# Optimization experiments

Hardware: AMD Instinct MI355X
Metric: run time of the kernel (lower is better)

Reference implementation:

```python
import jax, jax.numpy as jnp
import numpy as np

B = 4096      # batch (number of graphs / query nodes)
N = 524288    # total ball nodes (~128 per graph)
H = 128       # hidden_dim


def setup_inputs() -> dict:
    key = jax.random.key(0)
    ks = jax.random.split(key, 12)
    s = 0.05
    return {
        "query": jax.random.normal(ks[0], (B, H), dtype=jnp.float32),
        "ball": jax.random.normal(ks[1], (N, H), dtype=jnp.float32),
        "ball_batch": jnp.sort(jax.random.randint(ks[2], (N,), 0, B, dtype=jnp.int32)),
        # ball_attention: Linear(H, H//2) -> Tanh -> Linear(H//2, 1)
        "attn_w1": jax.random.normal(ks[3], (H, H // 2), dtype=jnp.float32) * s,
        "attn_b1": jnp.zeros((H // 2,), dtype=jnp.float32),
        "attn_w2": jax.random.normal(ks[4], (H // 2, 1), dtype=jnp.float32) * s,
        "attn_b2": jnp.zeros((1,), dtype=jnp.float32),
        # combiner: Linear(2H, H) -> LayerNorm(H) -> GELU
        "comb_w": jax.random.normal(ks[5], (2 * H, H), dtype=jnp.float32) * s,
        "comb_b": jnp.zeros((H,), dtype=jnp.float32),
        "ln_g": jnp.ones((H,), dtype=jnp.float32),
        "ln_b": jnp.zeros((H,), dtype=jnp.float32),
        # boundary head: Linear(H, H//2) -> ReLU -> Linear(H//2, 1)
        "bnd_w1": jax.random.normal(ks[6], (H, H // 2), dtype=jnp.float32) * s,
        "bnd_b1": jnp.zeros((H // 2,), dtype=jnp.float32),
        "bnd_w2": jax.random.normal(ks[7], (H // 2, 1), dtype=jnp.float32) * s,
        "bnd_b2": jnp.zeros((1,), dtype=jnp.float32),
        # wicket head: Linear(H, H//2) -> ReLU -> Linear(H//2, 1)
        "wkt_w1": jax.random.normal(ks[8], (H, H // 2), dtype=jnp.float32) * s,
        "wkt_b1": jnp.zeros((H // 2,), dtype=jnp.float32),
        "wkt_w2": jax.random.normal(ks[9], (H // 2, 1), dtype=jnp.float32) * s,
        "wkt_b2": jnp.zeros((1,), dtype=jnp.float32),
    }


def reference(query, ball, ball_batch, attn_w1, attn_b1, attn_w2, attn_b2,
              comb_w, comb_b, ln_g, ln_b,
              bnd_w1, bnd_b1, bnd_w2, bnd_b2,
              wkt_w1, wkt_b1, wkt_w2, wkt_b2):
    nb = query.shape[0]  # static batch size
    # attention score MLP over ball nodes -> [N]
    scores = (jnp.tanh(ball @ attn_w1 + attn_b1) @ attn_w2 + attn_b2)[:, 0]
    # segment softmax (stable: subtract per-segment max)
    seg_max = jax.ops.segment_max(scores, ball_batch, num_segments=nb)
    e = jnp.exp(scores - seg_max[ball_batch])
    denom = jax.ops.segment_sum(e, ball_batch, num_segments=nb)
    w = e / denom[ball_batch]
    # weighted-sum pooling -> [B, H]
    pooled = jax.ops.segment_sum(w[:, None] * ball, ball_batch, num_segments=nb)
    # concat + combiner: Linear -> LayerNorm -> GELU (exact, torch default)
    h = jnp.concatenate([query, pooled], axis=-1) @ comb_w + comb_b
    mu = jnp.mean(h, axis=-1, keepdims=True)
    var = jnp.mean((h - mu) ** 2, axis=-1, keepdims=True)
    h = (h - mu) / jnp.sqrt(var + 1e-5) * ln_g + ln_b
    h = jax.nn.gelu(h, approximate=False)
    boundary = jax.nn.relu(h @ bnd_w1 + bnd_b1) @ bnd_w2 + bnd_b2
    wicket = jax.nn.relu(h @ wkt_w1 + wkt_b1) @ wkt_w2 + wkt_b2
    return boundary, wicket
```

## Files before the change

kernel.cpp:

```cpp
#include <hip/hip_runtime.h>
#include <math.h>

#define N_NODES 524288
#define BATCH   4096
#define HID     128
#define MAXL    512

typedef __attribute__((ext_vector_type(8))) short bf16x8;
typedef __attribute__((ext_vector_type(4))) float f32x4;

__device__ __forceinline__ unsigned short f2bf(float f) {
  unsigned int u = __float_as_uint(f);
  u = (u + 0x7FFFu + ((u >> 16) & 1u)) >> 16;
  return (unsigned short)u;
}

__device__ __forceinline__ float fast_tanh(float x) {
  float cx = fminf(fmaxf(x, -9.f), 9.f);
  float e  = __expf(2.f * cx);
  return (e - 1.f) * __builtin_amdgcn_rcpf(e + 1.f);
}

__global__ __launch_bounds__(256) void k_bounds(const int* __restrict__ bb,
                                                int* __restrict__ rs)
{
  const int i = blockIdx.x * 256 + threadIdx.x;
  if (i >= N_NODES) return;
  const int cur  = bb[i];
  const int prev = (i == 0) ? -1 : bb[i - 1];
  for (int b = prev + 1; b <= cur; ++b) rs[b] = i;
  if (i == N_NODES - 1)
    for (int b = cur + 1; b <= BATCH; ++b) rs[b] = N_NODES;
}

__global__ __launch_bounds__(256, 8) void k_score_pool(
    const float* __restrict__ ball, const int* __restrict__ rs,
    const float* __restrict__ w1, const float* __restrict__ b1,
    const float* __restrict__ w2, const float* __restrict__ b2,
    float* __restrict__ pooled)
{
  __shared__ float  s_part[4][MAXL];
  __shared__ float  s_red[4];
  __shared__ float4 s_red4[3][32];

  const int tid  = threadIdx.x;
  const int lane = tid & 63;
  const int wv   = tid >> 6;
  const int m16  = lane & 15;
  const int quad = lane >> 4;
  const int b    = blockIdx.x;

  const int start = rs[b];
  const int end   = rs[b + 1];
  int L = end - start;

  float4* outp = (float4*)(pooled + (size_t)b * HID);
  if (L <= 0) { if (tid < 32) outp[tid] = make_float4(0.f,0.f,0.f,0.f); return; }
  if (L > MAXL) L = MAXL;

  bf16x8 fb[4];
  const int n = wv * 16 + m16;
  #pragma unroll
  for (int s = 0; s < 4; ++s) {
    const int k0 = s * 32 + quad * 8;
    bf16x8 v;
    #pragma unroll
    for (int j = 0; j < 8; ++j) v[j] = (short)f2bf(w1[(k0 + j) * 64 + n]);
    fb[s] = v;
  }
  const float b1v = b1[n], w2v = w2[n];

  for (int t0 = 0; t0 < L; t0 += 16) {
    int row = start + t0 + m16;
    if (row >= end) row = end - 1;
    const float4* rp = (const float4*)(ball + (size_t)row * HID) + quad * 2;
    f32x4 acc = {0.f, 0.f, 0.f, 0.f};
    #pragma unroll
    for (int s = 0; s < 4; ++s) {
      float4 x0 = rp[s * 8], x1 = rp[s * 8 + 1];
      bf16x8 fa;
      fa[0]=(short)f2bf(x0.x); fa[1]=(short)f2bf(x0.y);
      fa[2]=(short)f2bf(x0.z); fa[3]=(short)f2bf(x0.w);
      fa[4]=(short)f2bf(x1.x); fa[5]=(short)f2bf(x1.y);
      fa[6]=(short)f2bf(x1.z); fa[7]=(short)f2bf(x1.w);
      acc = __builtin_amdgcn_mfma_f32_16x16x32_bf16(fa, fb[s], acc, 0,0,0);
    }
    #pragma unroll
    for (int r = 0; r < 4; ++r) {
      float p = fast_tanh(acc[r] + b1v) * w2v;
      p += __shfl_xor(p, 1); p += __shfl_xor(p, 2);
      p += __shfl_xor(p, 4); p += __shfl_xor(p, 8);
      const int idx = t0 + quad * 4 + r;
      if (m16 == 0 && idx < L) s_part[wv][idx] = p;
    }
    __syncthreads();
  }
  __syncthreads();

  float m = -INFINITY;
  for (int i = lane; i < L; i += 64)
    m = fmaxf(m, s_part[0][i] + s_part[1][i] + s_part[2][i] + s_part[3][i]);
  #pragma unroll
  for (int o = 32; o; o >>= 1) m = fmaxf(m, __shfl_xor(m, o));
  __syncthreads();

  float d = 0.f;
  for (int i = wv * 64 + lane; i < L; i += 256) {
    float e = __expf(s_part[0][i] + s_part[1][i] + s_part[2][i] + s_part[3][i] - m);
    s_part[0][i] = e;
    d += e;
  }
  #pragma unroll
  for (int o = 32; o; o >>= 1) d += __shfl_xor(d, o);
  if (lane == 0) s_red[wv] = d;
  __syncthreads();
  const float inv = __builtin_amdgcn_rcpf(s_red[0] + s_red[1] + s_red[2] + s_red[3]);

  const int lh = lane >> 5;
  const int c4 = lane & 31;
  float4 acc = {0.f, 0.f, 0.f, 0.f};
  #pragma unroll 4
  for (int i = start + wv * 2; i + 1 < end; i += 8) {
    const int   row = i + lh;
    const float w   = s_part[0][row - start];
    const float4 v  = ((const float4*)(ball + (size_t)row * HID))[c4];
    acc.x = fmaf(w, v.x, acc.x);
    acc.y = fmaf(w, v.y, acc.y);
    acc.z = fmaf(w, v.z, acc.z);
    acc.w = fmaf(w, v.w, acc.w);
  }
  if ((L & 1) && wv == 0 && lh == 0) {
    const int   row = end - 1;
    const float w   = s_part[0][row - start];
    const float4 v  = ((const float4*)(ball + (size_t)row * HID))[c4];
    acc.x = fmaf(w, v.x, acc.x);
    acc.y = fmaf(w, v.y, acc.y);
    acc.z = fmaf(w, v.z, acc.z);
    acc.w = fmaf(w, v.w, acc.w);
  }
  acc.x += __shfl_xor(acc.x, 32);
  acc.y += __shfl_xor(acc.y, 32);
  acc.z += __shfl_xor(acc.z, 32);
  acc.w += __shfl_xor(acc.w, 32);
  if (wv != 0) { if (lh == 0) s_red4[wv - 1][c4] = acc; }
  __syncthreads();
  if (wv == 0 && lh == 0) {
    const float4 a1 = s_red4[0][c4], a2 = s_red4[1][c4], a3 = s_red4[2][c4];
    float4 o;
    o.x = (acc.x + a1.x + a2.x + a3.x) * inv;
    o.y = (acc.y + a1.y + a2.y + a3.y) * inv;
    o.z = (acc.z + a1.z + a2.z + a3.z) * inv;
    o.w = (acc.w + a1.w + a2.w + a3.w) * inv;
    outp[c4] = o;
  }
}

__global__ __launch_bounds__(128) void k_combine(
    const float* __restrict__ query, const float* __restrict__ pooled,
    const float* __restrict__ cw, const float* __restrict__ cb,
    const float* __restrict__ lg, const float* __restrict__ lb,
    const float* __restrict__ bw1, const float* __restrict__ bb1,
    const float* __restrict__ bw2, const float* __restrict__ bb2,
    const float* __restrict__ ww1, const float* __restrict__ wb1,
    const float* __restrict__ ww2, const float* __restrict__ wb2,
    float* __restrict__ out)
{
  __shared__ float in_lds[256][8];
  __shared__ float h_lds[128][8];
  __shared__ float part[2][2][8];
  const int tid  = threadIdx.x;
  const int row0 = blockIdx.x * 8;

  for (int idx = tid; idx < 2048; idx += 128) {
    const int k = idx >> 3, r = idx & 7;
    float v = (k < 128) ? query[(size_t)(row0 + r) * 128 + k]
                        : pooled[(size_t)(row0 + r) * 128 + (k - 128)];
    in_lds[k][r] = v;
  }
  __syncthreads();

  const int j = tid;
  float acc[8];
  const float cbj = cb[j];
  #pragma unroll
  for (int r = 0; r < 8; ++r) acc[r] = cbj;
  for (int k = 0; k < 256; ++k) {
    const float w = cw[k * 128 + j];
    #pragma unroll
    for (int r = 0; r < 8; ++r) acc[r] = fmaf(in_lds[k][r], w, acc[r]);
  }

  const int wv = tid >> 6, ln = tid & 63;
  #pragma unroll
  for (int r = 0; r < 8; ++r) {
    float v = acc[r], v2 = v * v;
    #pragma unroll
    for (int o = 32; o; o >>= 1) { v += __shfl_xor(v, o); v2 += __shfl_xor(v2, o); }
    if (ln == 0) { part[0][wv][r] = v; part[1][wv][r] = v2; }
  }
  __syncthreads();
  const float gj = lg[j], bj = lb[j];
  #pragma unroll
  for (int r = 0; r < 8; ++r) {
    const float S = part[0][0][r] + part[0][1][r];
    const float Q = part[1][0][r] + part[1][1][r];
    const float mean = S * (1.f / 128.f);
    const float var  = Q * (1.f / 128.f) - mean * mean;
    const float rs   = rsqrtf(var + 1e-5f);
    float x = (acc[r] - mean) * rs * gj + bj;
    x = 0.5f * x * (1.f + erff(x * 0.70710678118654752f));
    h_lds[j][r] = x;
  }
  __syncthreads();

  const float* W1 = wv ? ww1 : bw1;
  const float* B1 = wv ? wb1 : bb1;
  const float* W2 = wv ? ww2 : bw2;
  const float  B2 = wv ? wb2[0] : bb2[0];
  float t[8];
  const float b1l = B1[ln];
  #pragma unroll
  for (int r = 0; r < 8; ++r) t[r] = b1l;
  for (int k = 0; k < 128; ++k) {
    const float w = W1[k * 64 + ln];
    #pragma unroll
    for (int r = 0; r < 8; ++r) t[r] = fmaf(h_lds[k][r], w, t[r]);
  }
  const float w2l = W2[ln];
  #pragma unroll
  for (int r = 0; r < 8; ++r) {
    float o = fmaxf(t[r], 0.f) * w2l;
    #pragma unroll
    for (int m = 32; m; m >>= 1) o += __shfl_xor(o, m);
    if (ln == 0) out[wv * BATCH + row0 + r] = o + B2;
  }
}

extern "C" void kernel_launch(void* const* d_in, const int* in_sizes, int n_in,
                              void* d_out, int out_size, void* d_ws, size_t ws_size,
                              hipStream_t stream)
{
  const float* query = (const float*)d_in[0];
  const float* ball  = (const float*)d_in[1];
  const int*   bb    = (const int*)  d_in[2];
  const float* aw1   = (const float*)d_in[3];
  const float* ab1   = (const float*)d_in[4];
  const float* aw2   = (const float*)d_in[5];
  const float* ab2   = (const float*)d_in[6];
  const float* cw    = (const float*)d_in[7];
  const float* cb    = (const float*)d_in[8];
  const float* lg    = (const float*)d_in[9];
  const float* lbeta = (const float*)d_in[10];
  const float* bw1   = (const float*)d_in[11];
  const float* bb1   = (const float*)d_in[12];
  const float* bw2   = (const float*)d_in[13];
  const float* bb2   = (const float*)d_in[14];
  const float* ww1   = (const float*)d_in[15];
  const float* wb1   = (const float*)d_in[16];
  const float* ww2   = (const float*)d_in[17];
  const float* wb2   = (const float*)d_in[18];

  float* pooled = (float*)d_ws;
  int*   rs     = (int*)(pooled + (size_t)BATCH * HID);
  float* out    = (float*)d_out;

  k_bounds<<<(N_NODES + 255) / 256, 256, 0, stream>>>(bb, rs);
  k_score_pool<<<BATCH, 256, 0, stream>>>(ball, rs, aw1, ab1, aw2, ab2, pooled);
  k_combine<<<BATCH / 8, 128, 0, stream>>>(query, pooled, cw, cb, lg, lbeta,
                                           bw1, bb1, bw2, bb2, ww1, wb1, ww2, wb2, out);
}
```

Baseline: 488.2 us.

## Stage ball rows in swizzled LDS with double buffering and online softmax

Restructures the score+pool kernel so each segment's ball rows are loaded from global memory once, in 32-row chunks, into a double-buffered, XOR-swizzled LDS tile. Both the MFMA scoring and the weighted pooling read from that tile, with an online running-max softmax replacing the separate max/sum/pool passes. This removes the second global read of every ball row and the MAXL cap on segment length. In exchange it uses about 32KB of LDS per block, which lowers occupancy, and adds extra barriers per chunk.

```diff
diff --git a/kernel.cpp b/kernel.cpp
--- a/kernel.cpp
+++ b/kernel.cpp
@@ -4,7 +4,7 @@
 #define N_NODES 524288
 #define BATCH   4096
 #define HID     128
-#define MAXL    512
+#define CH      32
 
 typedef __attribute__((ext_vector_type(8))) short bf16x8;
 typedef __attribute__((ext_vector_type(4))) float f32x4;
@@ -20,6 +20,8 @@
   float e  = __expf(2.f * cx);
   return (e - 1.f) * __builtin_amdgcn_rcpf(e + 1.f);
 }
+
+#define SWZ(row, col) (((row) * HID) + ((((col) >> 2) ^ ((row) & 7)) << 2) + ((col) & 3))
 
 __global__ __launch_bounds__(256) void k_bounds(const int* __restrict__ bb,
                                                 int* __restrict__ rs)
@@ -33,15 +35,16 @@
     for (int b = cur + 1; b <= BATCH; ++b) rs[b] = N_NODES;
 }
 
-__global__ __launch_bounds__(256, 8) void k_score_pool(
+__global__ __launch_bounds__(256) void k_score_pool(
     const float* __restrict__ ball, const int* __restrict__ rs,
     const float* __restrict__ w1, const float* __restrict__ b1,
     const float* __restrict__ w2, const float* __restrict__ b2,
     float* __restrict__ pooled)
 {
-  __shared__ float  s_part[4][MAXL];
-  __shared__ float  s_red[4];
-  __shared__ float4 s_red4[3][32];
+  __shared__ __align__(16) float buf[2][CH * HID];
+  __shared__ float s_part[4][CH];
+  __shared__ float s_red[4];
+  __shared__ float s_obuf[3][HID];
 
   const int tid  = threadIdx.x;
   const int lane = tid & 63;
@@ -52,11 +55,10 @@
 
   const int start = rs[b];
   const int end   = rs[b + 1];
-  int L = end - start;
-
-  float4* outp = (float4*)(pooled + (size_t)b * HID);
-  if (L <= 0) { if (tid < 32) outp[tid] = make_float4(0.f,0.f,0.f,0.f); return; }
-  if (L > MAXL) L = MAXL;
+  const int L     = end - start;
+
+  float2* outp = (float2*)(pooled + (size_t)b * HID);
+  if (L <= 0) { if (tid < 64) outp[tid] = make_float2(0.f, 0.f); return; }
 
   bf16x8 fb[4];
   const int n = wv * 16 + m16;
@@ -70,88 +72,107 @@
   }
   const float b1v = b1[n], w2v = w2[n];
 
-  for (int t0 = 0; t0 < L; t0 += 16) {
-    int row = start + t0 + m16;
-    if (row >= end) row = end - 1;
-    const float4* rp = (const float4*)(ball + (size_t)row * HID) + quad * 2;
-    f32x4 acc = {0.f, 0.f, 0.f, 0.f};
-    #pragma unroll
-    for (int s = 0; s < 4; ++s) {
-      float4 x0 = rp[s * 8], x1 = rp[s * 8 + 1];
-      bf16x8 fa;
-      fa[0]=(short)f2bf(x0.x); fa[1]=(short)f2bf(x0.y);
-      fa[2]=(short)f2bf(x0.z); fa[3]=(short)f2bf(x0.w);
-      fa[4]=(short)f2bf(x1.x); fa[5]=(short)f2bf(x1.y);
-      fa[6]=(short)f2bf(x1.z); fa[7]=(short)f2bf(x1.w);
-      acc = __builtin_amdgcn_mfma_f32_16x16x32_bf16(fa, fb[s], acc, 0,0,0);
-    }
-    #pragma unroll
-    for (int r = 0; r < 4; ++r) {
-      float p = fast_tanh(acc[r] + b1v) * w2v;
-      p += __shfl_xor(p, 1); p += __shfl_xor(p, 2);
-      p += __shfl_xor(p, 4); p += __shfl_xor(p, 8);
-      const int idx = t0 + quad * 4 + r;
-      if (m16 == 0 && idx < L) s_part[wv][idx] = p;
+  const int nc = (L + CH - 1) / CH;
+  float4 pre[4];
+
+  #pragma unroll
+  for (int rnd = 0; rnd < 4; ++rnd) {
+    const int f = rnd * 1024 + tid * 4;
+    const int row = f >> 7, col = f & 127;
+    int gr = start + row; if (gr >= end) gr = end - 1;
+    pre[rnd] = *(const float4*)(ball + (size_t)gr * HID + col);
+  }
+  #pragma unroll
+  for (int rnd = 0; rnd < 4; ++rnd) {
+    const int f = rnd * 1024 + tid * 4;
+    const int row = f >> 7, col = f & 127;
+    *(float4*)&buf[0][SWZ(row, col)] = pre[rnd];
+  }
+  __syncthreads();
+
+  float  m_run = -INFINITY, d_run = 0.f;
+  float2 O = make_float2(0.f, 0.f);
+  int p = 0;
+
+  for (int c = 0; c < nc; ++c) {
+    const int Lc = min(CH, L - c * CH);
+
+    if (c + 1 < nc) {
+      #pragma unroll
+      for (int rnd = 0; rnd < 4; ++rnd) {
+        const int f = rnd * 1024 + tid * 4;
+        const int row = f >> 7, col = f & 127;
+        int gr = start + (c + 1) * CH + row; if (gr >= end) gr = end - 1;
+        pre[rnd] = *(const float4*)(ball + (size_t)gr * HID + col);
+      }
+    }
+
+    #pragma unroll
+    for (int sub = 0; sub < 2; ++sub) {
+      const int row = sub * 16 + m16;
+      f32x4 acc = {0.f, 0.f, 0.f, 0.f};
+      #pragma unroll
+      for (int s = 0; s < 4; ++s) {
+        const float4 x0 = *(const float4*)&buf[p][SWZ(row, s * 32 + quad * 8)];
+        const float4 x1 = *(const float4*)&buf[p][SWZ(row, s * 32 + quad * 8 + 4)];
+        bf16x8 fa;
+        fa[0]=(short)f2bf(x0.x); fa[1]=(short)f2bf(x0.y);
+        fa[2]=(short)f2bf(x0.z); fa[3]=(short)f2bf(x0.w);
+        fa[4]=(short)f2bf(x1.x); fa[5]=(short)f2bf(x1.y);
+        fa[6]=(short)f2bf(x1.z); fa[7]=(short)f2bf(x1.w);
+        acc = __builtin_amdgcn_mfma_f32_16x16x32_bf16(fa, fb[s], acc, 0,0,0);
+      }
+      #pragma unroll
+      for (int r = 0; r < 4; ++r) {
+        float sc = fast_tanh(acc[r] + b1v) * w2v;
+        sc += __shfl_xor(sc, 1); sc += __shfl_xor(sc, 2);
+        sc += __shfl_xor(sc, 4); sc += __shfl_xor(sc, 8);
+        if (m16 == 0) s_part[wv][sub * 16 + quad * 4 + r] = sc;
+      }
     }
     __syncthreads();
-  }
-  __syncthreads();
-
-  float m = -INFINITY;
-  for (int i = lane; i < L; i += 64)
-    m = fmaxf(m, s_part[0][i] + s_part[1][i] + s_part[2][i] + s_part[3][i]);
-  #pragma unroll
-  for (int o = 32; o; o >>= 1) m = fmaxf(m, __shfl_xor(m, o));
-  __syncthreads();
-
-  float d = 0.f;
-  for (int i = wv * 64 + lane; i < L; i += 256) {
-    float e = __expf(s_part[0][i] + s_part[1][i] + s_part[2][i] + s_part[3][i] - m);
-    s_part[0][i] = e;
-    d += e;
-  }
-  #pragma unroll
-  for (int o = 32; o; o >>= 1) d += __shfl_xor(d, o);
-  if (lane == 0) s_red[wv] = d;
-  __syncthreads();
-  const float inv = __builtin_amdgcn_rcpf(s_red[0] + s_red[1] + s_red[2] + s_red[3]);
-
-  const int lh = lane >> 5;
-  const int c4 = lane & 31;
-  float4 acc = {0.f, 0.f, 0.f, 0.f};
-  #pragma unroll 4
-  for (int i = start + wv * 2; i + 1 < end; i += 8) {
-    const int   row = i + lh;
-    const float w   = s_part[0][row - start];
-    const float4 v  = ((const float4*)(ball + (size_t)row * HID))[c4];
-    acc.x = fmaf(w, v.x, acc.x);
-    acc.y = fmaf(w, v.y, acc.y);
-    acc.z = fmaf(w, v.z, acc.z);
-    acc.w = fmaf(w, v.w, acc.w);
-  }
-  if ((L & 1) && wv == 0 && lh == 0) {
-    const int   row = end - 1;
-    const float w   = s_part[0][row - start];
-    const float4 v  = ((const float4*)(ball + (size_t)row * HID))[c4];
-    acc.x = fmaf(w, v.x, acc.x);
-    acc.y = fmaf(w, v.y, acc.y);
-    acc.z = fmaf(w, v.z, acc.z);
-    acc.w = fmaf(w, v.w, acc.w);
-  }
-  acc.x += __shfl_xor(acc.x, 32);
-  acc.y += __shfl_xor(acc.y, 32);
-  acc.z += __shfl_xor(acc.z, 32);
-  acc.w += __shfl_xor(acc.w, 32);
-  if (wv != 0) { if (lh == 0) s_red4[wv - 1][c4] = acc; }
-  __syncthreads();
-  if (wv == 0 && lh == 0) {
-    const float4 a1 = s_red4[0][c4], a2 = s_red4[1][c4], a3 = s_red4[2][c4];
-    float4 o;
-    o.x = (acc.x + a1.x + a2.x + a3.x) * inv;
-    o.y = (acc.y + a1.y + a2.y + a3.y) * inv;
-    o.z = (acc.z + a1.z + a2.z + a3.z) * inv;
-    o.w = (acc.w + a1.w + a2.w + a3.w) * inv;
-    outp[c4] = o;
+
+    const float sv = (lane < Lc)
+        ? (s_part[0][lane] + s_part[1][lane] + s_part[2][lane] + s_part[3][lane])
+        : -INFINITY;
+    float mc = sv;
+    #pragma unroll
+    for (int o = 32; o; o >>= 1) mc = fmaxf(mc, __shfl_xor(mc, o));
+    const float m_new = fmaxf(m_run, mc);
+    const float scale = __expf(m_run - m_new);
+    d_run *= scale; O.x *= scale; O.y *= scale;
+    m_run = m_new;
+
+    if (c + 1 < nc) {
+      #pragma unroll
+      for (int rnd = 0; rnd < 4; ++rnd) {
+        const int f = rnd * 1024 + tid * 4;
+        const int row = f >> 7, col = f & 127;
+        *(float4*)&buf[p ^ 1][SWZ(row, col)] = pre[rnd];
+      }
+    }
+
+    for (int r = wv; r < Lc; r += 4) {
+      const float e = __expf(__shfl(sv, r) - m_new);
+      const float2 v = *(const float2*)
+          &buf[p][r * HID + (((lane >> 1) ^ (r & 7)) << 2) + (lane & 1) * 2];
+      O.x = fmaf(e, v.x, O.x);
+      O.y = fmaf(e, v.y, O.y);
+      d_run += e;
+    }
+    __syncthreads();
+    p ^= 1;
+  }
+
+  if (wv) { s_obuf[wv - 1][lane * 2] = O.x; s_obuf[wv - 1][lane * 2 + 1] = O.y; }
+  if (lane == 0) s_red[wv] = d_run;
+  __syncthreads();
+  if (wv == 0) {
+    const float inv = 1.f / (s_red[0] + s_red[1] + s_red[2] + s_red[3]);
+    float2 o;
+    o.x = (O.x + s_obuf[0][lane*2]   + s_obuf[1][lane*2]   + s_obuf[2][lane*2])   * inv;
+    o.y = (O.y + s_obuf[0][lane*2+1] + s_obuf[1][lane*2+1] + s_obuf[2][lane*2+1]) * inv;
+    outp[lane] = o;
   }
 }
 
@@ -206,8 +227,8 @@
     const float Q = part[1][0][r] + part[1][1][r];
     const float mean = S * (1.f / 128.f);
     const float var  = Q * (1.f / 128.f) - mean * mean;
-    const float rs   = rsqrtf(var + 1e-5f);
-    float x = (acc[r] - mean) * rs * gj + bj;
+    const float rsd  = rsqrtf(var + 1e-5f);
+    float x = (acc[r] - mean) * rsd * gj + bj;
     x = 0.5f * x * (1.f + erff(x * 0.70710678118654752f));
     h_lds[j][r] = x;
   }
```

Measured after the change: 481.6 us. About the same (-1.4%).
